# Kernel optimization log

Hardware: AMD Instinct MI355X
Metric: run time of the kernel (lower is better)

The kernel has to match this reference:

```python
import jax, jax.numpy as jnp
import numpy as np

N_NODES = 50000
K_SAMPLE = 16  # ceil(32 * threshold 0.5)
# calculate_theta2(d=2): Beta-wavelet polynomial coeffs (ascending powers of L)
THETAS = [(3.0, -3.0, 0.75), (0.0, 3.0, -1.5), (0.0, 0.0, 0.75)]
AGG_WEIGHT = (0.0, 1.0)


def setup_inputs() -> dict:
    key = jax.random.key(0)
    ks = jax.random.split(key, 12)
    inp = {}
    inp['feat_table'] = jax.random.normal(ks[0], (N_NODES, 128), jnp.float32)
    inp['Wclf'] = jax.random.normal(ks[1], (128, 2), jnp.float32) * 0.05
    inp['bclf'] = jnp.zeros((2,), jnp.float32)
    inp['W1'] = jax.random.normal(ks[2], (128, 64), jnp.float32) * 0.05
    inp['b1'] = jnp.zeros((64,), jnp.float32)
    inp['W2'] = jax.random.normal(ks[3], (64, 64), jnp.float32) * 0.05
    inp['b2'] = jnp.zeros((64,), jnp.float32)
    inp['W3'] = jax.random.normal(ks[4], (64, 128), jnp.float32) * 0.05
    inp['b3'] = jnp.zeros((128,), jnp.float32)
    inp['weight'] = jax.random.normal(ks[5], (128, 64), jnp.float32) * 0.05
    inp['nodes'] = jax.random.randint(ks[6], (8192,), 0, N_NODES)
    inp['r1_neighs'] = jax.random.randint(ks[7], (8192, 32), 0, N_NODES)
    inp['edge_src'] = jax.random.randint(ks[8], (1600000,), 0, N_NODES)
    inp['edge_dst'] = jax.random.randint(ks[9], (1600000,), 0, N_NODES)
    return inp


def reference(feat_table, Wclf, bclf, W1, b1, W2, b2, W3, b3, weight,
              nodes, r1_neighs, edge_src, edge_dst):
    n = nodes.shape[0]
    embed_dim = W1.shape[1]

    # label scores for ALL nodes (label_clf over full feature table)
    batch_scores = feat_table @ Wclf + bclf                    # [N, 2]
    center_scores = batch_scores[nodes]                        # [n, 2]

    # ---- intra-relation agg (CARE-GNN style neighbor filtering) ----
    # distance on class-1 softmax prob, keep K_SAMPLE closest neighbors, mean-pool features
    center_p = jax.nn.softmax(center_scores, axis=-1)[:, 1]    # [n]
    neigh_scores = batch_scores[r1_neighs]                     # [n, D, 2]
    neigh_p = jax.nn.softmax(neigh_scores, axis=-1)[:, :, 1]   # [n, D]
    dist = jnp.abs(neigh_p - center_p[:, None])                # [n, D]
    _, sel = jax.lax.top_k(-dist, K_SAMPLE)                    # [n, K]
    sel_neighs = jnp.take_along_axis(r1_neighs, sel, axis=1)   # [n, K]
    r1_feats = jnp.mean(feat_table[sel_neighs], axis=1)        # [n, feat_dim]

    # ---- spectral branch (BWGNN PolyConv chain over the full graph) ----
    deg = jax.ops.segment_sum(jnp.ones_like(edge_dst, dtype=jnp.float32),
                              edge_dst, num_segments=N_NODES)
    dinv = jax.lax.rsqrt(jnp.maximum(deg, 1.0))                # [N]

    def lap(f):  # L f = f - D^{-1/2} A D^{-1/2} f
        s = f * dinv[:, None]
        agg = jax.ops.segment_sum(s[edge_src], edge_dst, num_segments=N_NODES)
        return f - agg * dinv[:, None]

    h = jax.nn.relu(feat_table @ W1 + b1)
    h = jax.nn.relu(h @ W2 + b2)                               # [N, embed]
    for theta in THETAS:  # convs applied sequentially, as in the source
        Lh = lap(h)
        L2h = lap(Lh)
        h = theta[0] * h + theta[1] * Lh + theta[2] * L2h
    h = h @ W3 + b3                                            # [N, feat_dim]
    spe_feats = h[nodes]                                       # [n, feat_dim]

    # ---- threshold_inter_agg (Eq. 9), agg_weight = [0, 1] ----
    self_feats = feat_table[nodes]
    center_h = self_feats @ weight                             # [n, embed]
    aggregated = AGG_WEIGHT[0] * (r1_feats @ weight) + AGG_WEIGHT[1] * (spe_feats @ weight)
    combined = jax.nn.relu(center_h + aggregated)              # [n, embed]
    return combined, center_scores
```

## Files before the change

### kernel.cpp

```cpp
#include <hip/hip_runtime.h>

#define FEAT 128
#define EMB 64
#define NB 256

typedef unsigned short u16;

__device__ inline u16 f2bf(float f) {
    unsigned u = __float_as_uint(f);
    unsigned r = (u + 0x7FFFu + ((u >> 16) & 1u)) >> 16;
    return (u16)r;
}
__device__ inline unsigned pack2(float lo, float hi) {
    return ((unsigned)f2bf(hi) << 16) | (unsigned)f2bf(lo);
}
__device__ inline void acc8(float* acc, uint4 v) {
    acc[0] += __uint_as_float(v.x << 16);
    acc[1] += __uint_as_float(v.x & 0xFFFF0000u);
    acc[2] += __uint_as_float(v.y << 16);
    acc[3] += __uint_as_float(v.y & 0xFFFF0000u);
    acc[4] += __uint_as_float(v.z << 16);
    acc[5] += __uint_as_float(v.z & 0xFFFF0000u);
    acc[6] += __uint_as_float(v.w << 16);
    acc[7] += __uint_as_float(v.w & 0xFFFF0000u);
}


__global__ __launch_bounds__(256) void hist_kernel(const int* __restrict__ edge_dst,
        int* __restrict__ table, int n_edges, int nbuck, int chunk) {
    __shared__ int hist[256];
    int t = threadIdx.x, b = blockIdx.x;
    hist[t] = 0;
    __syncthreads();
    int start = b * chunk, end = min(start + chunk, n_edges);
    for (int e = start + t; e < end; e += 256) {
        int d = __builtin_nontemporal_load(&edge_dst[e]);
        atomicAdd(&hist[d >> 8], 1);
    }
    __syncthreads();
    if (t < nbuck) table[t * NB + b] = hist[t];
}

__global__ void block_sum_kernel(const int* __restrict__ v, int* __restrict__ bsum, int n) {
    __shared__ int sd[256];
    int t = threadIdx.x;
    int i = blockIdx.x * 256 + t;
    sd[t] = (i < n) ? v[i] : 0;
    __syncthreads();
    for (int off = 128; off > 0; off >>= 1) {
        if (t < off) sd[t] += sd[t + off];
        __syncthreads();
    }
    if (t == 0) bsum[blockIdx.x] = sd[0];
}

__global__ void scan_bsum_kernel(const int* __restrict__ bsum, int* __restrict__ boff, int nb) {
    __shared__ int sd[256];
    int t = threadIdx.x;
    int v = (t < nb) ? bsum[t] : 0;
    sd[t] = v;
    __syncthreads();
    for (int off = 1; off < 256; off <<= 1) {
        int u = (t >= off) ? sd[t - off] : 0;
        __syncthreads();
        sd[t] += u;
        __syncthreads();
    }
    if (t < nb) boff[t] = sd[t] - v;
}

__global__ void scan_table_kernel(const int* __restrict__ tin, const int* __restrict__ boff,
                                  int* __restrict__ tout, int n) {
    __shared__ int sd[256];
    int t = threadIdx.x;
    int i = blockIdx.x * 256 + t;
    int v = (i < n) ? tin[i] : 0;
    sd[t] = v;
    __syncthreads();
    for (int off = 1; off < 256; off <<= 1) {
        int u = (t >= off) ? sd[t - off] : 0;
        __syncthreads();
        sd[t] += u;
        __syncthreads();
    }
    if (i < n) tout[i] = boff[blockIdx.x] + sd[t] - v;
}

__global__ __launch_bounds__(256) void scatter_kernel(
        const int* __restrict__ edge_src, const int* __restrict__ edge_dst,
        const int* __restrict__ tscan, unsigned* __restrict__ pairs,
        int n_edges, int nbuck, int chunk) {
    __shared__ int cur[256];
    int t = threadIdx.x, b = blockIdx.x;
    if (t < nbuck) cur[t] = tscan[t * NB + b];
    __syncthreads();
    int start = b * chunk, end = min(start + chunk, n_edges);
    for (int e = start + t; e < end; e += 256) {
        int d = __builtin_nontemporal_load(&edge_dst[e]);
        int s = __builtin_nontemporal_load(&edge_src[e]);
        int pos = atomicAdd(&cur[d >> 8], 1);
        pairs[pos] = ((unsigned)(d & 255) << 16) | (unsigned)s;
    }
}

__global__ __launch_bounds__(256) void finalize_kernel(
        const unsigned* __restrict__ pairs, const int* __restrict__ boff,
        int* __restrict__ rowptr, float* __restrict__ dinv, u16* __restrict__ csr,
        int n_edges, int N, int nbuck) {
    __shared__ int hist[256];
    __shared__ int scan[256];
    __shared__ int cur[256];
    int b = blockIdx.x, t = threadIdx.x;
    int node0 = b << 8;
    int base = boff[b];
    int end  = (b + 1 < nbuck) ? boff[b + 1] : n_edges;
    hist[t] = 0;
    __syncthreads();
    for (int p = base + t; p < end; p += 256)
        atomicAdd(&hist[pairs[p] >> 16], 1);
    __syncthreads();
    int v = hist[t];
    scan[t] = v;
    __syncthreads();
    for (int off = 1; off < 256; off <<= 1) {
        int u = (t >= off) ? scan[t - off] : 0;
        __syncthreads();
        scan[t] += u;
        __syncthreads();
    }
    int excl = scan[t] - v;
    cur[t] = base + excl;
    int node = node0 + t;
    if (node < N) {
        rowptr[node] = base + excl;
        dinv[node] = rsqrtf(fmaxf((float)v, 1.0f));
    }
    if (b == 0 && t == 0) rowptr[N] = n_edges;
    __syncthreads();
    for (int p = base + t; p < end; p += 256) {
        unsigned pr = pairs[p];
        int pos = atomicAdd(&cur[pr >> 16], 1);
        csr[pos] = (u16)(pr & 0xFFFFu);
    }
}


__global__ __launch_bounds__(256) void mlp_kernel(const float* __restrict__ feat,
        const float* __restrict__ W1, const float* __restrict__ b1,
        const float* __restrict__ W2, const float* __restrict__ b2,
        const float* __restrict__ dinv,
        float* __restrict__ A, u16* __restrict__ Ay, int n) {
    __shared__ float sBuf[32 * FEAT];
    int tid = threadIdx.x;
    int row0 = blockIdx.x * 32;

    for (int i = tid; i < 32 * FEAT; i += 256) {
        int r = i >> 7, c = i & 127;
        int gr = row0 + r;
        int s = c >> 2;
        int idx = r * FEAT + (((s ^ ((r >> 1) & 7)) << 2) | (c & 3));
        sBuf[idx] = (gr < n) ? feat[(size_t)gr * FEAT + c] : 0.0f;
    }
    __syncthreads();

    int tx = tid & 15, ty = tid >> 4;
    float4 b1v = *(const float4*)&b1[tx * 4];
    float acc[2][4];
    #pragma unroll
    for (int i = 0; i < 2; ++i) { acc[i][0]=b1v.x; acc[i][1]=b1v.y; acc[i][2]=b1v.z; acc[i][3]=b1v.w; }

    #pragma unroll 4
    for (int k4 = 0; k4 < FEAT / 4; ++k4) {
        float4 a4[2];
        #pragma unroll
        for (int i = 0; i < 2; ++i) {
            int r = ty * 2 + i;
            a4[i] = *(const float4*)&sBuf[r * FEAT + ((k4 ^ (ty & 7)) << 2)];
        }
        #pragma unroll
        for (int kk = 0; kk < 4; ++kk) {
            float4 bv = *(const float4*)&W1[(k4 * 4 + kk) * EMB + tx * 4];
            #pragma unroll
            for (int i = 0; i < 2; ++i) {
                float a = ((const float*)&a4[i])[kk];
                acc[i][0] = fmaf(a, bv.x, acc[i][0]);
                acc[i][1] = fmaf(a, bv.y, acc[i][1]);
                acc[i][2] = fmaf(a, bv.z, acc[i][2]);
                acc[i][3] = fmaf(a, bv.w, acc[i][3]);
            }
        }
    }
    __syncthreads();

    float* sH = sBuf;
    #pragma unroll
    for (int i = 0; i < 2; ++i) {
        int r = ty * 2 + i;
        float4 hv;
        hv.x = fmaxf(acc[i][0], 0.0f); hv.y = fmaxf(acc[i][1], 0.0f);
        hv.z = fmaxf(acc[i][2], 0.0f); hv.w = fmaxf(acc[i][3], 0.0f);
        *(float4*)&sH[r * EMB + ((tx ^ (ty & 7)) << 2)] = hv;
    }
    __syncthreads();

    float4 b2v = *(const float4*)&b2[tx * 4];
    float acc2[2][4];
    #pragma unroll
    for (int i = 0; i < 2; ++i) { acc2[i][0]=b2v.x; acc2[i][1]=b2v.y; acc2[i][2]=b2v.z; acc2[i][3]=b2v.w; }

    #pragma unroll 4
    for (int k4 = 0; k4 < EMB / 4; ++k4) {
        float4 a4[2];
        #pragma unroll
        for (int i = 0; i < 2; ++i) {
            int r = ty * 2 + i;
            a4[i] = *(const float4*)&sH[r * EMB + ((k4 ^ (ty & 7)) << 2)];
        }
        #pragma unroll
        for (int kk = 0; kk < 4; ++kk) {
            float4 bv = *(const float4*)&W2[(k4 * 4 + kk) * EMB + tx * 4];
            #pragma unroll
            for (int i = 0; i < 2; ++i) {
                float a = ((const float*)&a4[i])[kk];
                acc2[i][0] = fmaf(a, bv.x, acc2[i][0]);
                acc2[i][1] = fmaf(a, bv.y, acc2[i][1]);
                acc2[i][2] = fmaf(a, bv.z, acc2[i][2]);
                acc2[i][3] = fmaf(a, bv.w, acc2[i][3]);
            }
        }
    }

    #pragma unroll
    for (int i = 0; i < 2; ++i) {
        int gr = row0 + ty * 2 + i;
        if (gr < n) {
            float di = dinv[gr];
            float4 o;
            o.x = fmaxf(acc2[i][0], 0.0f); o.y = fmaxf(acc2[i][1], 0.0f);
            o.z = fmaxf(acc2[i][2], 0.0f); o.w = fmaxf(acc2[i][3], 0.0f);
            *(float4*)&A[(size_t)gr * EMB + tx * 4] = o;
            uint2 oy;
            oy.x = pack2(o.x * di, o.y * di);
            oy.y = pack2(o.z * di, o.w * di);
            *(uint2*)&Ay[(size_t)gr * EMB + tx * 4] = oy;
        }
    }
}


__global__ __launch_bounds__(256) void lap_kernel(
        const float4* __restrict__ x, const uint4* __restrict__ y,
        float4* __restrict__ Bx, uint4* __restrict__ By,
        const int* __restrict__ rowptr, const u16* __restrict__ csr,
        const float* __restrict__ dinv, int n) {
    int tid = blockIdx.x * blockDim.x + threadIdx.x;
    int g = tid >> 3, gl = tid & 7;
    if (g >= n) return;
    int s = rowptr[g], e = rowptr[g + 1];
    float acc[8] = {0.f,0.f,0.f,0.f,0.f,0.f,0.f,0.f};
    int p = s;
    for (; p + 7 < e; p += 8) {
        int i0 = csr[p],   i1 = csr[p+1], i2 = csr[p+2], i3 = csr[p+3];
        int i4 = csr[p+4], i5 = csr[p+5], i6 = csr[p+6], i7 = csr[p+7];
        uint4 v0 = y[(size_t)i0 * 8 + gl];
        uint4 v1 = y[(size_t)i1 * 8 + gl];
        uint4 v2 = y[(size_t)i2 * 8 + gl];
        uint4 v3 = y[(size_t)i3 * 8 + gl];
        uint4 v4 = y[(size_t)i4 * 8 + gl];
        uint4 v5 = y[(size_t)i5 * 8 + gl];
        uint4 v6 = y[(size_t)i6 * 8 + gl];
        uint4 v7 = y[(size_t)i7 * 8 + gl];
        acc8(acc, v0); acc8(acc, v1); acc8(acc, v2); acc8(acc, v3);
        acc8(acc, v4); acc8(acc, v5); acc8(acc, v6); acc8(acc, v7);
    }
    for (; p < e; ++p) {
        int i0 = csr[p];
        acc8(acc, y[(size_t)i0 * 8 + gl]);
    }
    float di = dinv[g];
    float4 xa = x[(size_t)g * 16 + gl * 2];
    float4 xb = x[(size_t)g * 16 + gl * 2 + 1];
    float4 oa, ob;
    oa.x = xa.x - acc[0] * di; oa.y = xa.y - acc[1] * di;
    oa.z = xa.z - acc[2] * di; oa.w = xa.w - acc[3] * di;
    ob.x = xb.x - acc[4] * di; ob.y = xb.y - acc[5] * di;
    ob.z = xb.z - acc[6] * di; ob.w = xb.w - acc[7] * di;
    Bx[(size_t)g * 16 + gl * 2] = oa;
    Bx[(size_t)g * 16 + gl * 2 + 1] = ob;
    uint4 oy;
    oy.x = pack2(oa.x * di, oa.y * di);
    oy.y = pack2(oa.z * di, oa.w * di);
    oy.z = pack2(ob.x * di, ob.y * di);
    oy.w = pack2(ob.z * di, ob.w * di);
    By[(size_t)g * 8 + gl] = oy;
}

__global__ __launch_bounds__(256) void theta_kernel(
        float4* __restrict__ Ax, uint4* __restrict__ Ay,
        const float4* __restrict__ Bx, const uint4* __restrict__ By,
        const int* __restrict__ rowptr, const u16* __restrict__ csr,
        const float* __restrict__ dinv, int n, float t0, float t1, float t2, int skip_a) {
    int tid = blockIdx.x * blockDim.x + threadIdx.x;
    int g = tid >> 3, gl = tid & 7;
    if (g >= n) return;
    int s = rowptr[g], e = rowptr[g + 1];
    float acc[8] = {0.f,0.f,0.f,0.f,0.f,0.f,0.f,0.f};
    int p = s;
    for (; p + 7 < e; p += 8) {
        int i0 = csr[p],   i1 = csr[p+1], i2 = csr[p+2], i3 = csr[p+3];
        int i4 = csr[p+4], i5 = csr[p+5], i6 = csr[p+6], i7 = csr[p+7];
        uint4 v0 = By[(size_t)i0 * 8 + gl];
        uint4 v1 = By[(size_t)i1 * 8 + gl];
        uint4 v2 = By[(size_t)i2 * 8 + gl];
        uint4 v3 = By[(size_t)i3 * 8 + gl];
        uint4 v4 = By[(size_t)i4 * 8 + gl];
        uint4 v5 = By[(size_t)i5 * 8 + gl];
        uint4 v6 = By[(size_t)i6 * 8 + gl];
        uint4 v7 = By[(size_t)i7 * 8 + gl];
        acc8(acc, v0); acc8(acc, v1); acc8(acc, v2); acc8(acc, v3);
        acc8(acc, v4); acc8(acc, v5); acc8(acc, v6); acc8(acc, v7);
    }
    for (; p < e; ++p) {
        int i0 = csr[p];
        acc8(acc, By[(size_t)i0 * 8 + gl]);
    }
    float di = dinv[g];
    float4 ba = Bx[(size_t)g * 16 + gl * 2];
    float4 bb = Bx[(size_t)g * 16 + gl * 2 + 1];
    float4 aa = {0.f,0.f,0.f,0.f}, ab = {0.f,0.f,0.f,0.f};
    if (!skip_a) {
        aa = Ax[(size_t)g * 16 + gl * 2];
        ab = Ax[(size_t)g * 16 + gl * 2 + 1];
    }
    float4 oa, ob;
    oa.x = t0 * aa.x + t1 * ba.x + t2 * (ba.x - acc[0] * di);
    oa.y = t0 * aa.y + t1 * ba.y + t2 * (ba.y - acc[1] * di);
    oa.z = t0 * aa.z + t1 * ba.z + t2 * (ba.z - acc[2] * di);
    oa.w = t0 * aa.w + t1 * ba.w + t2 * (ba.w - acc[3] * di);
    ob.x = t0 * ab.x + t1 * bb.x + t2 * (bb.x - acc[4] * di);
    ob.y = t0 * ab.y + t1 * bb.y + t2 * (bb.y - acc[5] * di);
    ob.z = t0 * ab.z + t1 * bb.z + t2 * (bb.z - acc[6] * di);
    ob.w = t0 * ab.w + t1 * bb.w + t2 * (bb.w - acc[7] * di);
    Ax[(size_t)g * 16 + gl * 2] = oa;
    Ax[(size_t)g * 16 + gl * 2 + 1] = ob;
    uint4 oy;
    oy.x = pack2(oa.x * di, oa.y * di);
    oy.y = pack2(oa.z * di, oa.w * di);
    oy.z = pack2(ob.x * di, ob.y * di);
    oy.w = pack2(ob.z * di, ob.w * di);
    Ay[(size_t)g * 8 + gl] = oy;
}

__global__ __launch_bounds__(256) void theta_sel_kernel(
        const float4* __restrict__ Bx, const uint4* __restrict__ By,
        const int* __restrict__ rowptr, const u16* __restrict__ csr,
        const float* __restrict__ dinv, const int* __restrict__ nodes,
        float4* __restrict__ hsel, int n, float t2) {
    int tid = blockIdx.x * blockDim.x + threadIdx.x;
    int i = tid >> 3, gl = tid & 7;
    if (i >= n) return;
    int g = nodes[i];
    int s = rowptr[g], e = rowptr[g + 1];
    float acc[8] = {0.f,0.f,0.f,0.f,0.f,0.f,0.f,0.f};
    int p = s;
    for (; p + 7 < e; p += 8) {
        int i0 = csr[p],   i1 = csr[p+1], i2 = csr[p+2], i3 = csr[p+3];
        int i4 = csr[p+4], i5 = csr[p+5], i6 = csr[p+6], i7 = csr[p+7];
        uint4 v0 = By[(size_t)i0 * 8 + gl];
        uint4 v1 = By[(size_t)i1 * 8 + gl];
        uint4 v2 = By[(size_t)i2 * 8 + gl];
        uint4 v3 = By[(size_t)i3 * 8 + gl];
        uint4 v4 = By[(size_t)i4 * 8 + gl];
        uint4 v5 = By[(size_t)i5 * 8 + gl];
        uint4 v6 = By[(size_t)i6 * 8 + gl];
        uint4 v7 = By[(size_t)i7 * 8 + gl];
        acc8(acc, v0); acc8(acc, v1); acc8(acc, v2); acc8(acc, v3);
        acc8(acc, v4); acc8(acc, v5); acc8(acc, v6); acc8(acc, v7);
    }
    for (; p < e; ++p) acc8(acc, By[(size_t)csr[p] * 8 + gl]);
    float di = dinv[g];
    float4 ba = Bx[(size_t)g * 16 + gl * 2];
    float4 bb = Bx[(size_t)g * 16 + gl * 2 + 1];
    float4 oa, ob;
    oa.x = t2 * (ba.x - acc[0] * di); oa.y = t2 * (ba.y - acc[1] * di);
    oa.z = t2 * (ba.z - acc[2] * di); oa.w = t2 * (ba.w - acc[3] * di);
    ob.x = t2 * (bb.x - acc[4] * di); ob.y = t2 * (bb.y - acc[5] * di);
    ob.z = t2 * (bb.z - acc[6] * di); ob.w = t2 * (bb.w - acc[7] * di);
    hsel[(size_t)i * 16 + gl * 2] = oa;
    hsel[(size_t)i * 16 + gl * 2 + 1] = ob;
}


__global__ __launch_bounds__(256) void final1_kernel(const float* __restrict__ feat,
        const float* __restrict__ hsel, const float* __restrict__ W3, const float* __restrict__ b3,
        const float* __restrict__ Wclf, const float* __restrict__ bclf,
        const int* __restrict__ nodes, float* __restrict__ vtmp, float* __restrict__ scores,
        int n) {
    __shared__ float sHt[64 * 68];
    __shared__ float sWclf[FEAT * 2];
    __shared__ float sbclf[2];
    __shared__ int sNodes[64];
    int tid = threadIdx.x;
    int base = blockIdx.x * 64;

    for (int i = tid; i < FEAT * 2; i += 256) sWclf[i] = Wclf[i];
    if (tid < 2) sbclf[tid] = bclf[tid];
    if (tid < 64) {
        int gi = base + tid;
        sNodes[tid] = (gi < n) ? nodes[gi] : 0;
    }
    __syncthreads();
    for (int it = 0; it < 16; ++it) {
        int id = it * 256 + tid;
        int r = id >> 6, c = id & 63;
        int gi = base + r;
        sHt[r * 68 + c] = (gi < n) ? hsel[(size_t)gi * EMB + c] : 0.0f;
    }
    __syncthreads();

    {
        int wv = tid >> 6, ln = tid & 63;
        float bc0 = sbclf[0], bc1 = sbclf[1];
        for (int q = 0; q < 16; ++q) {
            int r = wv * 16 + q;
            int nd = sNodes[r];
            float f0 = feat[(size_t)nd * FEAT + ln];
            float f1 = feat[(size_t)nd * FEAT + 64 + ln];
            float p0 = f0 * sWclf[ln * 2]     + f1 * sWclf[(64 + ln) * 2];
            float p1 = f0 * sWclf[ln * 2 + 1] + f1 * sWclf[(64 + ln) * 2 + 1];
            #pragma unroll
            for (int off = 32; off > 0; off >>= 1) {
                p0 += __shfl_xor(p0, off);
                p1 += __shfl_xor(p1, off);
            }
            int gi = base + r;
            if (ln == 0 && gi < n) {
                scores[(size_t)gi * 2]     = p0 + bc0;
                scores[(size_t)gi * 2 + 1] = p1 + bc1;
            }
        }
    }

    int tx = tid & 31, ty = tid >> 5;
    float acc[8][4];
    #pragma unroll
    for (int i = 0; i < 8; ++i)
        #pragma unroll
        for (int j = 0; j < 4; ++j) acc[i][j] = 0.0f;

    #pragma unroll 2
    for (int k4 = 0; k4 < EMB / 4; ++k4) {
        float4 a4[8];
        #pragma unroll
        for (int i = 0; i < 8; ++i)
            a4[i] = *(const float4*)&sHt[(ty * 8 + i) * 68 + k4 * 4];
        #pragma unroll
        for (int kk = 0; kk < 4; ++kk) {
            float4 bv = *(const float4*)&W3[(k4 * 4 + kk) * FEAT + tx * 4];
            #pragma unroll
            for (int i = 0; i < 8; ++i) {
                float a = ((const float*)&a4[i])[kk];
                acc[i][0] = fmaf(a, bv.x, acc[i][0]);
                acc[i][1] = fmaf(a, bv.y, acc[i][1]);
                acc[i][2] = fmaf(a, bv.z, acc[i][2]);
                acc[i][3] = fmaf(a, bv.w, acc[i][3]);
            }
        }
    }

    float4 b3v = *(const float4*)&b3[tx * 4];
    #pragma unroll
    for (int i = 0; i < 8; ++i) {
        int r = ty * 8 + i;
        int gi = base + r;
        int nd = sNodes[r];
        float4 fv = *(const float4*)&feat[(size_t)nd * FEAT + tx * 4];
        float4 o;
        o.x = acc[i][0] + b3v.x + fv.x;
        o.y = acc[i][1] + b3v.y + fv.y;
        o.z = acc[i][2] + b3v.z + fv.z;
        o.w = acc[i][3] + b3v.w + fv.w;
        if (gi < n) *(float4*)&vtmp[(size_t)gi * FEAT + tx * 4] = o;
    }
}


__global__ __launch_bounds__(256) void final2_kernel(const float* __restrict__ vtmp,
        const float* __restrict__ weight, float* __restrict__ outc, int n) {
    __shared__ float sV[64 * FEAT];
    int tid = threadIdx.x;
    int base = blockIdx.x * 64;
    for (int i = tid; i < 64 * FEAT; i += 256) {
        int r = i >> 7, c = i & 127;
        int gi = base + r;
        int s = c >> 2;
        int idx = r * FEAT + (((s ^ ((r >> 2) & 7)) << 2) | (c & 3));
        sV[idx] = (gi < n) ? vtmp[(size_t)gi * FEAT + c] : 0.0f;
    }
    __syncthreads();

    int tx = tid & 15, ty = tid >> 4;
    float acc[4][4];
    #pragma unroll
    for (int i = 0; i < 4; ++i)
        #pragma unroll
        for (int j = 0; j < 4; ++j) acc[i][j] = 0.0f;

    #pragma unroll 4
    for (int k4 = 0; k4 < FEAT / 4; ++k4) {
        float4 a4[4];
        #pragma unroll
        for (int i = 0; i < 4; ++i) {
            int r = ty * 4 + i;
            a4[i] = *(const float4*)&sV[r * FEAT + ((k4 ^ (ty & 7)) << 2)];
        }
        #pragma unroll
        for (int kk = 0; kk < 4; ++kk) {
            float4 bv = *(const float4*)&weight[(k4 * 4 + kk) * EMB + tx * 4];
            #pragma unroll
            for (int i = 0; i < 4; ++i) {
                float a = ((const float*)&a4[i])[kk];
                acc[i][0] = fmaf(a, bv.x, acc[i][0]);
                acc[i][1] = fmaf(a, bv.y, acc[i][1]);
                acc[i][2] = fmaf(a, bv.z, acc[i][2]);
                acc[i][3] = fmaf(a, bv.w, acc[i][3]);
            }
        }
    }

    #pragma unroll
    for (int i = 0; i < 4; ++i) {
        int gi = base + ty * 4 + i;
        if (gi < n) {
            float4 o;
            o.x = fmaxf(acc[i][0], 0.0f); o.y = fmaxf(acc[i][1], 0.0f);
            o.z = fmaxf(acc[i][2], 0.0f); o.w = fmaxf(acc[i][3], 0.0f);
            *(float4*)&outc[(size_t)gi * EMB + tx * 4] = o;
        }
    }
}


extern "C" void kernel_launch(void* const* d_in, const int* in_sizes, int n_in,
                              void* d_out, int out_size, void* d_ws, size_t ws_size,
                              hipStream_t stream) {
    const float* feat   = (const float*)d_in[0];
    const float* Wclf   = (const float*)d_in[1];
    const float* bclf   = (const float*)d_in[2];
    const float* W1     = (const float*)d_in[3];
    const float* b1     = (const float*)d_in[4];
    const float* W2     = (const float*)d_in[5];
    const float* b2     = (const float*)d_in[6];
    const float* W3     = (const float*)d_in[7];
    const float* b3     = (const float*)d_in[8];
    const float* weight = (const float*)d_in[9];
    const int* nodes    = (const int*)d_in[10];
    const int* edge_src = (const int*)d_in[12];
    const int* edge_dst = (const int*)d_in[13];

    int n       = in_sizes[10];
    int n_edges = in_sizes[12];
    int N       = in_sizes[0] / FEAT;
    int nbuck   = (N + 255) >> 8;
    int chunk   = (n_edges + NB - 1) / NB;

    char* ws = (char*)d_ws;
    size_t off = 0;
    auto alloc = [&](size_t bytes) -> void* {
        void* p = ws + off;
        off = (off + bytes + 255) & ~(size_t)255;
        return p;
    };
    int*      table  = (int*)     alloc((size_t)nbuck * NB * 4);
    int*      tscan  = (int*)     alloc((size_t)nbuck * NB * 4);
    int*      bsum   = (int*)     alloc(256 * 4);
    int*      boff   = (int*)     alloc(256 * 4);
    int*      rowptr = (int*)     alloc((size_t)(N + 1) * 4);
    float*    dinv   = (float*)   alloc((size_t)N * 4);
    unsigned* pairs  = (unsigned*)alloc((size_t)n_edges * 4);
    u16*      csr    = (u16*)     alloc((size_t)n_edges * 2);
    float*    Axf    = (float*)   alloc((size_t)N * EMB * 4);
    u16*      Ayf    = (u16*)     alloc((size_t)N * EMB * 2);
    float*    Bxf    = (float*)   alloc((size_t)N * EMB * 4);
    u16*      Byf    = (u16*)     alloc((size_t)N * EMB * 2);
    float*    hsel   = (float*)   alloc((size_t)n * EMB * 4);
    float*    vtmp   = (float*)   alloc((size_t)n * FEAT * 4);

    float* out_combined = (float*)d_out;
    float* out_scores   = out_combined + (size_t)n * EMB;

    int L = nbuck * NB;
    hist_kernel<<<NB, 256, 0, stream>>>(edge_dst, table, n_edges, nbuck, chunk);
    block_sum_kernel<<<nbuck, 256, 0, stream>>>(table, bsum, L);
    scan_bsum_kernel<<<1, 256, 0, stream>>>(bsum, boff, nbuck);
    scan_table_kernel<<<nbuck, 256, 0, stream>>>(table, boff, tscan, L);
    scatter_kernel<<<NB, 256, 0, stream>>>(edge_src, edge_dst, tscan, pairs, n_edges, nbuck, chunk);
    finalize_kernel<<<nbuck, 256, 0, stream>>>(pairs, boff, rowptr, dinv, csr, n_edges, N, nbuck);

    int mb = (N + 31) / 32;
    mlp_kernel<<<mb, 256, 0, stream>>>(feat, W1, b1, W2, b2, dinv, Axf, Ayf, N);

    int lb = ((size_t)N * 8 + 255) / 256;
    lap_kernel<<<lb, 256, 0, stream>>>((const float4*)Axf, (const uint4*)Ayf,
                                       (float4*)Bxf, (uint4*)Byf, rowptr, csr, dinv, N);
    theta_kernel<<<lb, 256, 0, stream>>>((float4*)Axf, (uint4*)Ayf,
                                         (const float4*)Bxf, (const uint4*)Byf,
                                         rowptr, csr, dinv, N, 3.f, -3.f, 0.75f, 0);
    lap_kernel<<<lb, 256, 0, stream>>>((const float4*)Axf, (const uint4*)Ayf,
                                       (float4*)Bxf, (uint4*)Byf, rowptr, csr, dinv, N);
    theta_kernel<<<lb, 256, 0, stream>>>((float4*)Axf, (uint4*)Ayf,
                                         (const float4*)Bxf, (const uint4*)Byf,
                                         rowptr, csr, dinv, N, 0.f, 3.f, -1.5f, 1);
    lap_kernel<<<lb, 256, 0, stream>>>((const float4*)Axf, (const uint4*)Ayf,
                                       (float4*)Bxf, (uint4*)Byf, rowptr, csr, dinv, N);
    int selb = ((size_t)n * 8 + 255) / 256;
    theta_sel_kernel<<<selb, 256, 0, stream>>>((const float4*)Bxf, (const uint4*)Byf,
                                               rowptr, csr, dinv, nodes,
                                               (float4*)hsel, n, 0.75f);

    int fb = (n + 63) / 64;
    final1_kernel<<<fb, 256, 0, stream>>>(feat, hsel, W3, b3, Wclf, bclf, nodes,
                                          vtmp, out_scores, n);
    final2_kernel<<<fb, 256, 0, stream>>>(vtmp, weight, out_combined, n);
}
```

Baseline: 377.2 us.

## Use bf16 MFMA for the two-layer MLP with pre-packed weight fragments

The fp32 FMA shared-memory GEMMs for the W1/W2 MLP are replaced by bf16 MFMA 16x16x32 instructions, one wave per 16 rows. A small prep kernel converts and reorders W1/W2 into bf16 fragment layout. Features are rounded to bf16 in registers, so the LDS staging of the input tile goes away. This cuts ALU time in the MLP stage but lowers precision and writes outputs with scalar, less coalesced stores.

Result: faster. 342.3 us (-9.2%).

```diff
diff --git a/kernel.cpp b/kernel.cpp
--- a/kernel.cpp
+++ b/kernel.cpp
@@ -5,6 +5,8 @@
 #define NB 256
 
 typedef unsigned short u16;
+typedef __attribute__((ext_vector_type(8))) short bf16x8;
+typedef __attribute__((ext_vector_type(4))) float f32x4;
 
 __device__ inline u16 f2bf(float f) {
     unsigned u = __float_as_uint(f);
@@ -145,104 +147,92 @@
 }
 
 
+__global__ __launch_bounds__(256) void wprep_kernel(const float* __restrict__ W1,
+        const float* __restrict__ W2, u16* __restrict__ W1t, u16* __restrict__ W2t) {
+    int t = blockIdx.x * 256 + threadIdx.x;
+    if (t < 16 * 64 * 8) {
+        int j = t & 7, c = (t >> 3) & 63, kb = t >> 9;
+        W1t[t] = f2bf(W1[(kb * 8 + j) * EMB + c]);
+    }
+    if (t < 8 * 64 * 8) {
+        int j = t & 7, c = (t >> 3) & 63, kb = t >> 9;
+        W2t[t] = f2bf(W2[(kb * 8 + j) * EMB + c]);
+    }
+}
+
+
 __global__ __launch_bounds__(256) void mlp_kernel(const float* __restrict__ feat,
-        const float* __restrict__ W1, const float* __restrict__ b1,
-        const float* __restrict__ W2, const float* __restrict__ b2,
+        const u16* __restrict__ W1t, const float* __restrict__ b1,
+        const u16* __restrict__ W2t, const float* __restrict__ b2,
         const float* __restrict__ dinv,
         float* __restrict__ A, u16* __restrict__ Ay, int n) {
-    __shared__ float sBuf[32 * FEAT];
+    __shared__ u16 sH[4][16 * 72];
     int tid = threadIdx.x;
-    int row0 = blockIdx.x * 32;
-
-    for (int i = tid; i < 32 * FEAT; i += 256) {
-        int r = i >> 7, c = i & 127;
-        int gr = row0 + r;
-        int s = c >> 2;
-        int idx = r * FEAT + (((s ^ ((r >> 1) & 7)) << 2) | (c & 3));
-        sBuf[idx] = (gr < n) ? feat[(size_t)gr * FEAT + c] : 0.0f;
-    }
-    __syncthreads();
-
-    int tx = tid & 15, ty = tid >> 4;
-    float4 b1v = *(const float4*)&b1[tx * 4];
-    float acc[2][4];
-    #pragma unroll
-    for (int i = 0; i < 2; ++i) { acc[i][0]=b1v.x; acc[i][1]=b1v.y; acc[i][2]=b1v.z; acc[i][3]=b1v.w; }
-
-    #pragma unroll 4
-    for (int k4 = 0; k4 < FEAT / 4; ++k4) {
-        float4 a4[2];
-        #pragma unroll
-        for (int i = 0; i < 2; ++i) {
-            int r = ty * 2 + i;
-            a4[i] = *(const float4*)&sBuf[r * FEAT + ((k4 ^ (ty & 7)) << 2)];
-        }
-        #pragma unroll
-        for (int kk = 0; kk < 4; ++kk) {
-            float4 bv = *(const float4*)&W1[(k4 * 4 + kk) * EMB + tx * 4];
-            #pragma unroll
-            for (int i = 0; i < 2; ++i) {
-                float a = ((const float*)&a4[i])[kk];
-                acc[i][0] = fmaf(a, bv.x, acc[i][0]);
-                acc[i][1] = fmaf(a, bv.y, acc[i][1]);
-                acc[i][2] = fmaf(a, bv.z, acc[i][2]);
-                acc[i][3] = fmaf(a, bv.w, acc[i][3]);
+    int w = tid >> 6, l = tid & 63;
+    int lo = l & 15, hi = l >> 4;
+    int row0 = blockIdx.x * 64 + w * 16;
+
+    bf16x8 afr[4];
+    int arow = min(row0 + lo, n - 1);
+    const float* fbase = feat + (size_t)arow * FEAT + hi * 8;
+    #pragma unroll
+    for (int ks = 0; ks < 4; ++ks) {
+        float4 p0 = *(const float4*)(fbase + ks * 32);
+        float4 p1 = *(const float4*)(fbase + ks * 32 + 4);
+        bf16x8 a;
+        a[0] = (short)f2bf(p0.x); a[1] = (short)f2bf(p0.y);
+        a[2] = (short)f2bf(p0.z); a[3] = (short)f2bf(p0.w);
+        a[4] = (short)f2bf(p1.x); a[5] = (short)f2bf(p1.y);
+        a[6] = (short)f2bf(p1.z); a[7] = (short)f2bf(p1.w);
+        afr[ks] = a;
+    }
+
+    #pragma unroll
+    for (int ct = 0; ct < 4; ++ct) {
+        f32x4 acc = {0.f, 0.f, 0.f, 0.f};
+        #pragma unroll
+        for (int ks = 0; ks < 4; ++ks) {
+            bf16x8 b = *(const bf16x8*)&W1t[((ks * 4 + hi) * 64 + ct * 16 + lo) * 8];
+            acc = __builtin_amdgcn_mfma_f32_16x16x32_bf16(afr[ks], b, acc, 0, 0, 0);
+        }
+        int col = ct * 16 + lo;
+        float bias = b1[col];
+        #pragma unroll
+        for (int r = 0; r < 4; ++r) {
+            float h = fmaxf(acc[r] + bias, 0.f);
+            sH[w][(hi * 4 + r) * 72 + col] = f2bf(h);
+        }
+    }
+    __syncthreads();
+
+    bf16x8 a2[2];
+    #pragma unroll
+    for (int ks = 0; ks < 2; ++ks)
+        a2[ks] = *(const bf16x8*)&sH[w][lo * 72 + ks * 32 + hi * 8];
+
+    float dv[4];
+    #pragma unroll
+    for (int r = 0; r < 4; ++r)
+        dv[r] = dinv[min(row0 + hi * 4 + r, n - 1)];
+
+    #pragma unroll
+    for (int ct = 0; ct < 4; ++ct) {
+        f32x4 acc = {0.f, 0.f, 0.f, 0.f};
+        #pragma unroll
+        for (int ks = 0; ks < 2; ++ks) {
+            bf16x8 b = *(const bf16x8*)&W2t[((ks * 4 + hi) * 64 + ct * 16 + lo) * 8];
+            acc = __builtin_amdgcn_mfma_f32_16x16x32_bf16(a2[ks], b, acc, 0, 0, 0);
+        }
+        int col = ct * 16 + lo;
+        float bias = b2[col];
+        #pragma unroll
+        for (int r = 0; r < 4; ++r) {
+            int grow = row0 + hi * 4 + r;
+            if (grow < n) {
+                float o = fmaxf(acc[r] + bias, 0.f);
+                A[(size_t)grow * EMB + col] = o;
+                Ay[(size_t)grow * EMB + col] = f2bf(o * dv[r]);
             }
-        }
-    }
-    __syncthreads();
-
-    float* sH = sBuf;
-    #pragma unroll
-    for (int i = 0; i < 2; ++i) {
-        int r = ty * 2 + i;
-        float4 hv;
-        hv.x = fmaxf(acc[i][0], 0.0f); hv.y = fmaxf(acc[i][1], 0.0f);
-        hv.z = fmaxf(acc[i][2], 0.0f); hv.w = fmaxf(acc[i][3], 0.0f);
-        *(float4*)&sH[r * EMB + ((tx ^ (ty & 7)) << 2)] = hv;
-    }
-    __syncthreads();
-
-    float4 b2v = *(const float4*)&b2[tx * 4];
-    float acc2[2][4];
-    #pragma unroll
-    for (int i = 0; i < 2; ++i) { acc2[i][0]=b2v.x; acc2[i][1]=b2v.y; acc2[i][2]=b2v.z; acc2[i][3]=b2v.w; }
-
-    #pragma unroll 4
-    for (int k4 = 0; k4 < EMB / 4; ++k4) {
-        float4 a4[2];
-        #pragma unroll
-        for (int i = 0; i < 2; ++i) {
-            int r = ty * 2 + i;
-            a4[i] = *(const float4*)&sH[r * EMB + ((k4 ^ (ty & 7)) << 2)];
-        }
-        #pragma unroll
-        for (int kk = 0; kk < 4; ++kk) {
-            float4 bv = *(const float4*)&W2[(k4 * 4 + kk) * EMB + tx * 4];
-            #pragma unroll
-            for (int i = 0; i < 2; ++i) {
-                float a = ((const float*)&a4[i])[kk];
-                acc2[i][0] = fmaf(a, bv.x, acc2[i][0]);
-                acc2[i][1] = fmaf(a, bv.y, acc2[i][1]);
-                acc2[i][2] = fmaf(a, bv.z, acc2[i][2]);
-                acc2[i][3] = fmaf(a, bv.w, acc2[i][3]);
-            }
-        }
-    }
-
-    #pragma unroll
-    for (int i = 0; i < 2; ++i) {
-        int gr = row0 + ty * 2 + i;
-        if (gr < n) {
-            float di = dinv[gr];
-            float4 o;
-            o.x = fmaxf(acc2[i][0], 0.0f); o.y = fmaxf(acc2[i][1], 0.0f);
-            o.z = fmaxf(acc2[i][2], 0.0f); o.w = fmaxf(acc2[i][3], 0.0f);
-            *(float4*)&A[(size_t)gr * EMB + tx * 4] = o;
-            uint2 oy;
-            oy.x = pack2(o.x * di, o.y * di);
-            oy.y = pack2(o.z * di, o.w * di);
-            *(uint2*)&Ay[(size_t)gr * EMB + tx * 4] = oy;
         }
     }
 }
@@ -579,6 +569,8 @@
     float*    dinv   = (float*)   alloc((size_t)N * 4);
     unsigned* pairs  = (unsigned*)alloc((size_t)n_edges * 4);
     u16*      csr    = (u16*)     alloc((size_t)n_edges * 2);
+    u16*      W1t    = (u16*)     alloc(16 * 64 * 8 * 2);
+    u16*      W2t    = (u16*)     alloc(8 * 64 * 8 * 2);
     float*    Axf    = (float*)   alloc((size_t)N * EMB * 4);
     u16*      Ayf    = (u16*)     alloc((size_t)N * EMB * 2);
     float*    Bxf    = (float*)   alloc((size_t)N * EMB * 4);
@@ -590,6 +582,7 @@
     float* out_scores   = out_combined + (size_t)n * EMB;
 
     int L = nbuck * NB;
+    wprep_kernel<<<32, 256, 0, stream>>>(W1, W2, W1t, W2t);
     hist_kernel<<<NB, 256, 0, stream>>>(edge_dst, table, n_edges, nbuck, chunk);
     block_sum_kernel<<<nbuck, 256, 0, stream>>>(table, bsum, L);
     scan_bsum_kernel<<<1, 256, 0, stream>>>(bsum, boff, nbuck);
@@ -597,8 +590,8 @@
     scatter_kernel<<<NB, 256, 0, stream>>>(edge_src, edge_dst, tscan, pairs, n_edges, nbuck, chunk);
     finalize_kernel<<<nbuck, 256, 0, stream>>>(pairs, boff, rowptr, dinv, csr, n_edges, N, nbuck);
 
-    int mb = (N + 31) / 32;
-    mlp_kernel<<<mb, 256, 0, stream>>>(feat, W1, b1, W2, b2, dinv, Axf, Ayf, N);
+    int mb = (N + 63) / 64;
+    mlp_kernel<<<mb, 256, 0, stream>>>(feat, W1t, b1, W2t, b2, dinv, Axf, Ayf, N);
 
     int lb = ((size_t)N * 8 + 255) / 256;
     lap_kernel<<<lb, 256, 0, stream>>>((const float4*)Axf, (const uint4*)Ayf,
```
